# Performance work log

Measured on AMD Instinct MI355X. Metric: run time of the kernel, lower is better.

Reference implementation:

```python
import jax, jax.numpy as jnp
import numpy as np

N = 1024  # batch rows; each row has 480 features

def setup_inputs() -> dict:
    key = jax.random.key(0)
    kx, kS, kT, kH, kL = jax.random.split(key, 5)
    x = jax.random.normal(kx, (N, 480), dtype=jnp.float32)
    S = jax.random.normal(kS, (30, 2, 15), dtype=jnp.float32)    # buffer
    T = jax.random.normal(kT, (30, 15), dtype=jnp.float32)       # param
    H = jax.random.normal(kH, (45, 4096), dtype=jnp.float32)     # buffer (hash matrix)
    LUT = jax.random.normal(kL, (10, 4096, 2), dtype=jnp.float32)  # param (codebook)
    return {"x": x, "S": S, "T": T, "H": H, "LUT": LUT}

def reference(x, S, T, H, LUT):
    # (N, 480) -> (N, 8, 30, 2)
    x4 = x.reshape(-1, 8, 30, 2)
    # project each 2-vector through S: (N, 8, 30, 15)
    y = jnp.einsum('abcd,cdk->abck', x4, S) - T - 1e-4
    # straight-through sign-tanh binarization
    tanh = jnp.tanh(y)
    y = jax.lax.stop_gradient(jnp.sign(y) - tanh) + tanh
    # (N, 8, 10, 45): 30*15 = 10*(3*15)
    y = y.reshape(-1, 8, 10, 45)
    # hash scores over 4096 codes: (N, 8, 10, 4096)
    scores = jnp.einsum('bpcd,dk->bpck', y, H)
    idx = jnp.argmax(scores, axis=-1)  # (N, 8, 10) int
    # one_hot @ LUT is exactly a gather: out[b,p,c,:] = LUT[c, idx[b,p,c], :]
    out = LUT[jnp.arange(10)[None, None, :], idx]  # (N, 8, 10, 2)
    return out
```

## Files before the change

### kernel.cpp

```cpp
#include <hip/hip_runtime.h>
#include <math.h>

#define M_ROWS  81920
#define NCOLS   4096
#define KPAD    48
#define NCHUNK  4
#define CHUNKC  (NCOLS / NCHUNK)
#define CROUNDS (CHUNKC / 32)
#define GHALVES 3072
#define LO_SCALE 4096.0f
#define INV_LO   (1.0f / 4096.0f)

typedef _Float16 f16x8  __attribute__((ext_vector_type(8)));
typedef float    f32x16 __attribute__((ext_vector_type(16)));


__global__ void build_B_kernel(const float* __restrict__ H,
                               _Float16* __restrict__ Bfrag) {
    const int n = blockIdx.x * 256 + threadIdx.x;
    _Float16 hi[KPAD], lo[KPAD];
    #pragma unroll
    for (int k = 0; k < 45; ++k) {
        const float h = H[k * NCOLS + n];
        const _Float16 h1 = (_Float16)h;
        hi[k] = h1;
        lo[k] = (_Float16)((h - (float)h1) * LO_SCALE);
    }
    #pragma unroll
    for (int k = 45; k < KPAD; ++k) { hi[k] = (_Float16)0.f; lo[k] = (_Float16)0.f; }

    const int g = n >> 5;
    const int c = n & 31;
    _Float16* gbase = Bfrag + (size_t)g * GHALVES;
    #pragma unroll
    for (int f = 0; f < 6; ++f) {
        const int kt = (f < 3) ? f : f - 3;
        const _Float16* src = ((f < 3) ? hi : lo) + kt * 16;
        #pragma unroll
        for (int h = 0; h < 2; ++h) {
            *(f16x8*)(gbase + f * 512 + (h * 32 + c) * 8) =
                *(const f16x8*)(src + h * 8);
        }
    }
}

__global__ __launch_bounds__(512, 2) void score_argmax_kernel(
        const float* __restrict__ x,
        const float* __restrict__ S,
        const float* __restrict__ T,
        const _Float16* __restrict__ Bfrag,
        const float* __restrict__ LUT,
        float* __restrict__ out) {
    const int tid  = threadIdx.x;
    const int lane = tid & 63;
    const int l31  = lane & 31;
    const int half = lane >> 5;
    const int wid   = tid >> 6;
    const int chunk = wid & 3;
    const int rtile = wid >> 2;
    const int rowblk = blockIdx.x * 64;
    const int rowbase = rowblk + rtile * 32;

    __shared__ float lds_best[NCHUNK][64];
    __shared__ int   lds_bidx[NCHUNK][64];

    f16x8 afr[3];
    {
        const int row  = rowbase + l31;
        const int pair = row / 10;
        const int c2   = row - pair * 10;
        const int a    = pair >> 3;
        const int b    = pair & 7;
        const float* xp = x + a * 480 + b * 60;
        #pragma unroll
        for (int kt = 0; kt < 3; ++kt) {
            #pragma unroll
            for (int j = 0; j < 8; ++j) {
                const int k    = kt * 16 + half * 8 + j;
                const bool pad = (k >= 45);
                const int kcl  = pad ? 0 : k;
                const int cc   = kcl / 15;
                const int kk   = kcl - cc * 15;
                const int c    = c2 * 3 + cc;
                const float x0 = xp[c * 2 + 0];
                const float x1 = xp[c * 2 + 1];
                float v = x0 * S[(c * 2 + 0) * 15 + kk] + x1 * S[(c * 2 + 1) * 15 + kk];
                v = v - T[c * 15 + kk] - 1e-4f;
                const float yv = (v > 0.f) ? 1.f : ((v < 0.f) ? -1.f : 0.f);
                afr[kt][j] = pad ? (_Float16)0.f : (_Float16)yv;
            }
        }
    }

    float best[16];
    int   bidx[16];
    #pragma unroll
    for (int e = 0; e < 16; ++e) { best[e] = -INFINITY; bidx[e] = 0; }

    const int colbase0 = chunk * CHUNKC;
    const _Float16* fptr = Bfrag + (size_t)(colbase0 >> 5) * GHALVES + (size_t)lane * 8;

    for (int ct = 0; ct < CROUNDS; ++ct) {
        f16x8 cb[6];
        #pragma unroll
        for (int f = 0; f < 6; ++f) cb[f] = *(const f16x8*)(fptr + f * 512);

        f32x16 ch = {0.f};
        f32x16 cl = {0.f};
        ch = __builtin_amdgcn_mfma_f32_32x32x16_f16(afr[0], cb[0], ch, 0, 0, 0);
        ch = __builtin_amdgcn_mfma_f32_32x32x16_f16(afr[1], cb[1], ch, 0, 0, 0);
        ch = __builtin_amdgcn_mfma_f32_32x32x16_f16(afr[2], cb[2], ch, 0, 0, 0);
        cl = __builtin_amdgcn_mfma_f32_32x32x16_f16(afr[0], cb[3], cl, 0, 0, 0);
        cl = __builtin_amdgcn_mfma_f32_32x32x16_f16(afr[1], cb[4], cl, 0, 0, 0);
        cl = __builtin_amdgcn_mfma_f32_32x32x16_f16(afr[2], cb[5], cl, 0, 0, 0);

        const int mycol = colbase0 + ct * 32 + l31;
        #pragma unroll
        for (int e = 0; e < 16; ++e) {
            const float s = fmaf(cl[e], INV_LO, ch[e]);
            if (s > best[e]) bidx[e] = mycol;
            best[e] = fmaxf(best[e], s);
        }
        fptr += GHALVES;
    }

    #pragma unroll
    for (int m = 1; m < 32; m <<= 1) {
        #pragma unroll
        for (int e = 0; e < 16; ++e) {
            const float ov = __shfl_xor(best[e], m, 64);
            const int   oi = __shfl_xor(bidx[e], m, 64);
            if (ov > best[e] || (ov == best[e] && oi < bidx[e])) {
                best[e] = ov; bidx[e] = oi;
            }
        }
    }

    if (l31 == 0) {
        #pragma unroll
        for (int e = 0; e < 16; ++e) {
            const int r64 = rtile * 32 + (e & 3) + 8 * (e >> 2) + 4 * half;
            lds_best[chunk][r64] = best[e];
            lds_bidx[chunk][r64] = bidx[e];
        }
    }
    __syncthreads();

    if (tid < 64) {
        const int row = rowblk + tid;
        float bv = lds_best[0][tid];
        int   bi = lds_bidx[0][tid];
        #pragma unroll
        for (int c = 1; c < NCHUNK; ++c) {
            const float v = lds_best[c][tid];
            const int   i = lds_bidx[c][tid];
            if (v > bv) { bv = v; bi = i; }
        }
        const int pair = row / 10;
        const int c2   = row - pair * 10;
        const float* l = LUT + ((size_t)c2 * NCOLS + bi) * 2;
        out[row * 2 + 0] = l[0];
        out[row * 2 + 1] = l[1];
    }
}

extern "C" void kernel_launch(void* const* d_in, const int* in_sizes, int n_in,
                              void* d_out, int out_size, void* d_ws, size_t ws_size,
                              hipStream_t stream) {
    const float* x   = (const float*)d_in[0];
    const float* S   = (const float*)d_in[1];
    const float* T   = (const float*)d_in[2];
    const float* H   = (const float*)d_in[3];
    const float* LUT = (const float*)d_in[4];
    float* out = (float*)d_out;

    _Float16* Bfrag = (_Float16*)d_ws;

    build_B_kernel<<<16, 256, 0, stream>>>(H, Bfrag);
    score_argmax_kernel<<<1280, 512, 0, stream>>>(x, S, T, Bfrag, LUT, out);
}
```

Measured before the change: 182.6 us.

## Stage hash fragments through double-buffered LDS and give each wave all columns

Work is reorganised so that each wave covers 32 rows across all 4096 columns, in place of splitting columns into four chunks. This removes the cross-wave LDS reduction of per-chunk argmax results. Hash-matrix fragments are now loaded cooperatively from global memory into a double-buffered shared-memory tile. The next tile's global load is issued before the MFMAs on the current tile, so it can overlap with compute. The cost is a block barrier every iteration and fewer, smaller blocks (640×256 versus 1280×512).

```diff
diff --git a/kernel.cpp b/kernel.cpp
--- a/kernel.cpp
+++ b/kernel.cpp
@@ -4,10 +4,10 @@
 #define M_ROWS  81920
 #define NCOLS   4096
 #define KPAD    48
-#define NCHUNK  4
-#define CHUNKC  (NCOLS / NCHUNK)
-#define CROUNDS (CHUNKC / 32)
+#define CROUNDS 128
+#define ITERS   64
 #define GHALVES 3072
+#define ITBYTES 12288
 #define LO_SCALE 4096.0f
 #define INV_LO   (1.0f / 4096.0f)
 
@@ -44,7 +44,7 @@
     }
 }
 
-__global__ __launch_bounds__(512, 2) void score_argmax_kernel(
+__global__ __launch_bounds__(256, 4) void score_argmax_kernel(
         const float* __restrict__ x,
         const float* __restrict__ S,
         const float* __restrict__ T,
@@ -55,14 +55,10 @@
     const int lane = tid & 63;
     const int l31  = lane & 31;
     const int half = lane >> 5;
-    const int wid   = tid >> 6;
-    const int chunk = wid & 3;
-    const int rtile = wid >> 2;
-    const int rowblk = blockIdx.x * 64;
-    const int rowbase = rowblk + rtile * 32;
+    const int wid  = tid >> 6;
+    const int rowbase = blockIdx.x * 128 + wid * 32;
 
-    __shared__ float lds_best[NCHUNK][64];
-    __shared__ int   lds_bidx[NCHUNK][64];
+    __shared__ _Float16 sB[2][2 * GHALVES];
 
     f16x8 afr[3];
     {
@@ -97,32 +93,60 @@
     #pragma unroll
     for (int e = 0; e < 16; ++e) { best[e] = -INFINITY; bidx[e] = 0; }
 
-    const int colbase0 = chunk * CHUNKC;
-    const _Float16* fptr = Bfrag + (size_t)(colbase0 >> 5) * GHALVES + (size_t)lane * 8;
+    const char* gB = (const char*)Bfrag;
+    char* const lds0 = (char*)&sB[0][0];
+    char* const lds1 = (char*)&sB[1][0];
+    const size_t toff = (size_t)tid * 16;
 
-    for (int ct = 0; ct < CROUNDS; ++ct) {
-        f16x8 cb[6];
-        #pragma unroll
-        for (int f = 0; f < 6; ++f) cb[f] = *(const f16x8*)(fptr + f * 512);
+    f16x8 st[3];
 
-        f32x16 ch = {0.f};
-        f32x16 cl = {0.f};
-        ch = __builtin_amdgcn_mfma_f32_32x32x16_f16(afr[0], cb[0], ch, 0, 0, 0);
-        ch = __builtin_amdgcn_mfma_f32_32x32x16_f16(afr[1], cb[1], ch, 0, 0, 0);
-        ch = __builtin_amdgcn_mfma_f32_32x32x16_f16(afr[2], cb[2], ch, 0, 0, 0);
-        cl = __builtin_amdgcn_mfma_f32_32x32x16_f16(afr[0], cb[3], cl, 0, 0, 0);
-        cl = __builtin_amdgcn_mfma_f32_32x32x16_f16(afr[1], cb[4], cl, 0, 0, 0);
-        cl = __builtin_amdgcn_mfma_f32_32x32x16_f16(afr[2], cb[5], cl, 0, 0, 0);
+    #pragma unroll
+    for (int q = 0; q < 3; ++q)
+        st[q] = *(const f16x8*)(gB + (size_t)q * 4096 + toff);
+    #pragma unroll
+    for (int q = 0; q < 3; ++q)
+        *(f16x8*)(lds0 + q * 4096 + toff) = st[q];
+    __syncthreads();
 
-        const int mycol = colbase0 + ct * 32 + l31;
-        #pragma unroll
-        for (int e = 0; e < 16; ++e) {
-            const float s = fmaf(cl[e], INV_LO, ch[e]);
-            if (s > best[e]) bidx[e] = mycol;
-            best[e] = fmaxf(best[e], s);
-        }
-        fptr += GHALVES;
+#define ITER_BODY(rd, wr, it, itn) do {                                     \
+        _Pragma("unroll")                                                   \
+        for (int q = 0; q < 3; ++q)                                         \
+            st[q] = *(const f16x8*)(gB + (size_t)(itn) * ITBYTES            \
+                                       + (size_t)q * 4096 + toff);          \
+        _Pragma("unroll")                                                   \
+        for (int rr = 0; rr < 2; ++rr) {                                    \
+            const _Float16* fb = (const _Float16*)((rd) + rr * 6144)        \
+                                 + (size_t)lane * 8;                        \
+            f16x8 cb[6];                                                    \
+            _Pragma("unroll")                                               \
+            for (int f = 0; f < 6; ++f) cb[f] = *(const f16x8*)(fb + f * 512); \
+            f32x16 ch = {0.f};                                              \
+            f32x16 cl = {0.f};                                              \
+            ch = __builtin_amdgcn_mfma_f32_32x32x16_f16(afr[0], cb[0], ch, 0, 0, 0); \
+            ch = __builtin_amdgcn_mfma_f32_32x32x16_f16(afr[1], cb[1], ch, 0, 0, 0); \
+            ch = __builtin_amdgcn_mfma_f32_32x32x16_f16(afr[2], cb[2], ch, 0, 0, 0); \
+            cl = __builtin_amdgcn_mfma_f32_32x32x16_f16(afr[0], cb[3], cl, 0, 0, 0); \
+            cl = __builtin_amdgcn_mfma_f32_32x32x16_f16(afr[1], cb[4], cl, 0, 0, 0); \
+            cl = __builtin_amdgcn_mfma_f32_32x32x16_f16(afr[2], cb[5], cl, 0, 0, 0); \
+            const int mycol = ((it) * 2 + rr) * 32 + l31;                   \
+            _Pragma("unroll")                                               \
+            for (int e = 0; e < 16; ++e) {                                  \
+                const float s = fmaf(cl[e], INV_LO, ch[e]);                 \
+                if (s > best[e]) bidx[e] = mycol;          \
+                best[e] = fmaxf(best[e], s);                                \
+            }                                                               \
+        }                                                                   \
+        _Pragma("unroll")                                                   \
+        for (int q = 0; q < 3; ++q)                                         \
+            *(f16x8*)((wr) + q * 4096 + toff) = st[q];                      \
+        __syncthreads();                                                    \
+    } while (0)
+
+    for (int it2 = 0; it2 < ITERS; it2 += 2) {
+        ITER_BODY(lds0, lds1, it2,     it2 + 1);
+        ITER_BODY(lds1, lds0, it2 + 1, (it2 + 2) & (ITERS - 1));
     }
+#undef ITER_BODY
 
     #pragma unroll
     for (int m = 1; m < 32; m <<= 1) {
@@ -139,28 +163,13 @@
     if (l31 == 0) {
         #pragma unroll
         for (int e = 0; e < 16; ++e) {
-            const int r64 = rtile * 32 + (e & 3) + 8 * (e >> 2) + 4 * half;
-            lds_best[chunk][r64] = best[e];
-            lds_bidx[chunk][r64] = bidx[e];
+            const int row = rowbase + (e & 3) + 8 * (e >> 2) + 4 * half;
+            const int pair = row / 10;
+            const int c2   = row - pair * 10;
+            const float* l = LUT + ((size_t)c2 * NCOLS + bidx[e]) * 2;
+            out[row * 2 + 0] = l[0];
+            out[row * 2 + 1] = l[1];
         }
-    }
-    __syncthreads();
-
-    if (tid < 64) {
-        const int row = rowblk + tid;
-        float bv = lds_best[0][tid];
-        int   bi = lds_bidx[0][tid];
-        #pragma unroll
-        for (int c = 1; c < NCHUNK; ++c) {
-            const float v = lds_best[c][tid];
-            const int   i = lds_bidx[c][tid];
-            if (v > bv) { bv = v; bi = i; }
-        }
-        const int pair = row / 10;
-        const int c2   = row - pair * 10;
-        const float* l = LUT + ((size_t)c2 * NCOLS + bi) * 2;
-        out[row * 2 + 0] = l[0];
-        out[row * 2 + 1] = l[1];
     }
 }
 
@@ -177,5 +186,5 @@
     _Float16* Bfrag = (_Float16*)d_ws;
 
     build_B_kernel<<<16, 256, 0, stream>>>(H, Bfrag);
-    score_argmax_kernel<<<1280, 512, 0, stream>>>(x, S, T, Bfrag, LUT, out);
+    score_argmax_kernel<<<640, 256, 0, stream>>>(x, S, T, Bfrag, LUT, out);
 }
```

After: 232.9 us. 1.28x slower.

## Stage hash-matrix column chunk in LDS and merge chunk argmax via 64-bit atomics

Applied to the files above, without the earlier changes.

Each block now handles one of eight column chunks for 512 rows and copies that chunk's fp16 hi/lo fragments (96 KB) into shared memory once, so the MFMA loop reads B from LDS instead of repeatedly from global/L2. The per-block LDS cross-chunk reduction is replaced by packing score and index into a monotonic 64-bit key and using global atomicMax. A separate kernel then decodes the winning index and gathers from the LUT. This adds atomic traffic, a third kernel launch, and 1024-thread blocks at one block per CU, which may reduce latency hiding.

```diff
diff --git a/kernel.cpp b/kernel.cpp
--- a/kernel.cpp
+++ b/kernel.cpp
@@ -4,10 +4,11 @@
 #define M_ROWS  81920
 #define NCOLS   4096
 #define KPAD    48
-#define NCHUNK  4
+#define NCHUNK  8
 #define CHUNKC  (NCOLS / NCHUNK)
 #define CROUNDS (CHUNKC / 32)
 #define GHALVES 3072
+#define CHALVES (16 * GHALVES)
 #define LO_SCALE 4096.0f
 #define INV_LO   (1.0f / 4096.0f)
 
@@ -16,7 +17,8 @@
 
 
 __global__ void build_B_kernel(const float* __restrict__ H,
-                               _Float16* __restrict__ Bfrag) {
+                               _Float16* __restrict__ Bfrag,
+                               unsigned long long* __restrict__ keys) {
     const int n = blockIdx.x * 256 + threadIdx.x;
     _Float16 hi[KPAD], lo[KPAD];
     #pragma unroll
@@ -42,27 +44,26 @@
                 *(const f16x8*)(src + h * 8);
         }
     }
+    #pragma unroll
+    for (int i = 0; i < 20; ++i) keys[(size_t)n * 20 + i] = 0ull;
 }
 
-__global__ __launch_bounds__(512, 2) void score_argmax_kernel(
+__global__ __launch_bounds__(1024, 1) void score_argmax_kernel(
         const float* __restrict__ x,
         const float* __restrict__ S,
         const float* __restrict__ T,
         const _Float16* __restrict__ Bfrag,
-        const float* __restrict__ LUT,
-        float* __restrict__ out) {
+        unsigned long long* __restrict__ keys) {
     const int tid  = threadIdx.x;
     const int lane = tid & 63;
     const int l31  = lane & 31;
     const int half = lane >> 5;
-    const int wid   = tid >> 6;
-    const int chunk = wid & 3;
-    const int rtile = wid >> 2;
-    const int rowblk = blockIdx.x * 64;
-    const int rowbase = rowblk + rtile * 32;
+    const int wid  = tid >> 6;
+    const int chunk  = blockIdx.x / 160;
+    const int rowblk = blockIdx.x - chunk * 160;
+    const int rowbase = rowblk * 512 + wid * 32;
 
-    __shared__ float lds_best[NCHUNK][64];
-    __shared__ int   lds_bidx[NCHUNK][64];
+    __shared__ _Float16 sB[CHALVES];
 
     f16x8 afr[3];
     {
@@ -92,18 +93,28 @@
         }
     }
 
+    {
+        const _Float16* src = Bfrag + (size_t)chunk * CHALVES + (size_t)tid * 8;
+        _Float16* dst = sB + (size_t)tid * 8;
+        #pragma unroll
+        for (int p = 0; p < 6; ++p)
+            *(f16x8*)(dst + p * 8192) = *(const f16x8*)(src + p * 8192);
+    }
+    __syncthreads();
+
     float best[16];
     int   bidx[16];
     #pragma unroll
     for (int e = 0; e < 16; ++e) { best[e] = -INFINITY; bidx[e] = 0; }
 
     const int colbase0 = chunk * CHUNKC;
-    const _Float16* fptr = Bfrag + (size_t)(colbase0 >> 5) * GHALVES + (size_t)lane * 8;
+    const _Float16* lbase = sB + (size_t)lane * 8;
 
     for (int ct = 0; ct < CROUNDS; ++ct) {
+        const _Float16* fb = lbase + ct * GHALVES;
         f16x8 cb[6];
         #pragma unroll
-        for (int f = 0; f < 6; ++f) cb[f] = *(const f16x8*)(fptr + f * 512);
+        for (int f = 0; f < 6; ++f) cb[f] = *(const f16x8*)(fb + f * 512);
 
         f32x16 ch = {0.f};
         f32x16 cl = {0.f};
@@ -121,7 +132,6 @@
             if (s > best[e]) bidx[e] = mycol;
             best[e] = fmaxf(best[e], s);
         }
-        fptr += GHALVES;
     }
 
     #pragma unroll
@@ -139,29 +149,28 @@
     if (l31 == 0) {
         #pragma unroll
         for (int e = 0; e < 16; ++e) {
-            const int r64 = rtile * 32 + (e & 3) + 8 * (e >> 2) + 4 * half;
-            lds_best[chunk][r64] = best[e];
-            lds_bidx[chunk][r64] = bidx[e];
+            const int row = rowbase + (e & 3) + 8 * (e >> 2) + 4 * half;
+            const unsigned u = __float_as_uint(best[e]);
+            const unsigned mono = (u & 0x80000000u) ? ~u : (u | 0x80000000u);
+            const unsigned long long key =
+                ((unsigned long long)mono << 32) | (unsigned)(4095 - bidx[e]);
+            atomicMax(&keys[row], key);
         }
     }
-    __syncthreads();
+}
 
-    if (tid < 64) {
-        const int row = rowblk + tid;
-        float bv = lds_best[0][tid];
-        int   bi = lds_bidx[0][tid];
-        #pragma unroll
-        for (int c = 1; c < NCHUNK; ++c) {
-            const float v = lds_best[c][tid];
-            const int   i = lds_bidx[c][tid];
-            if (v > bv) { bv = v; bi = i; }
-        }
-        const int pair = row / 10;
-        const int c2   = row - pair * 10;
-        const float* l = LUT + ((size_t)c2 * NCOLS + bi) * 2;
-        out[row * 2 + 0] = l[0];
-        out[row * 2 + 1] = l[1];
-    }
+__global__ void reduce_lut_kernel(const unsigned long long* __restrict__ keys,
+                                  const float* __restrict__ LUT,
+                                  float* __restrict__ out) {
+    const int row = blockIdx.x * blockDim.x + threadIdx.x;
+    if (row >= M_ROWS) return;
+    const unsigned long long key = keys[row];
+    const int bi = 4095 - (int)(key & 0xFFFFFFFFull);
+    const int pair = row / 10;
+    const int c2   = row - pair * 10;
+    const float* l = LUT + ((size_t)c2 * NCOLS + bi) * 2;
+    out[row * 2 + 0] = l[0];
+    out[row * 2 + 1] = l[1];
 }
 
 extern "C" void kernel_launch(void* const* d_in, const int* in_sizes, int n_in,
@@ -175,7 +184,10 @@
     float* out = (float*)d_out;
 
     _Float16* Bfrag = (_Float16*)d_ws;
+    unsigned long long* keys =
+        (unsigned long long*)(Bfrag + (size_t)128 * GHALVES);
 
-    build_B_kernel<<<16, 256, 0, stream>>>(H, Bfrag);
-    score_argmax_kernel<<<1280, 512, 0, stream>>>(x, S, T, Bfrag, LUT, out);
+    build_B_kernel<<<16, 256, 0, stream>>>(H, Bfrag, keys);
+    score_argmax_kernel<<<1280, 1024, 0, stream>>>(x, S, T, Bfrag, keys);
+    reduce_lut_kernel<<<M_ROWS / 256, 256, 0, stream>>>(keys, LUT, out);
 }
```

Result: slower. 262.2 us (+43.6%).
